# Performance work log

Measured on AMD Instinct MI355X. Metric: run time of the kernel, lower is better.

## Reference

```python
import jax, jax.numpy as jnp
import numpy as np

# Screen config (matches init_kwargs)
W, H, TL = 1920, 1080, 16
NBW = -(-W // TL)          # 120
NBH = -(-H // TL)          # 68
NB = NBW * NBH             # 8160 tiles
N = 500_000                # number of points
K = 5                      # max tiles per axis a point can overlap (radius < 24, TL=16)
RADIUS_MAX = 24.0


def setup_inputs() -> dict:
    key = jax.random.key(0)
    k1, k2, k3 = jax.random.split(key, 3)
    pos2d = jax.random.uniform(k1, (N, 2), dtype=jnp.float32) * jnp.array([W, H], dtype=jnp.float32)
    radius = jax.random.uniform(k2, (N,), dtype=jnp.float32) * (RADIUS_MAX - 1.0) + 1.0
    depth = jax.random.normal(k3, (N,), dtype=jnp.float32)
    return {"pos2d": pos2d, "radius": radius, "depth": depth}


def reference(pos2d, radius, depth):
    # Tile bounds per point (identical clamping semantics to the torch module).
    xmin = jnp.clip(jnp.floor_divide(pos2d[:, 0] - radius, TL), 0, NBW).astype(jnp.int32)
    ymin = jnp.clip(jnp.floor_divide(pos2d[:, 1] - radius, TL), 0, NBH).astype(jnp.int32)
    xmax = jnp.clip(jnp.floor_divide(pos2d[:, 0] + radius, TL) + 1, 0, NBW).astype(jnp.int32)
    ymax = jnp.clip(jnp.floor_divide(pos2d[:, 1] + radius, TL) + 1, 0, NBH).astype(jnp.int32)

    # Enumerate a fixed KxK candidate tile window per point, mask out-of-range tiles.
    dxy = jnp.arange(K, dtype=jnp.int32)
    xi = xmin[:, None] + dxy            # [N, K]
    yi = ymin[:, None] + dxy            # [N, K]
    vx = xi < xmax[:, None]
    vy = yi < ymax[:, None]
    valid = (vx[:, :, None] & vy[:, None, :]).reshape(-1)              # [E]
    tid = (xi[:, :, None] * NBH + yi[:, None, :]).reshape(-1)          # [E] flat tile id (x-major, as in module)
    tid = jnp.where(valid, tid, NB).astype(jnp.int32)                  # sentinel NB -> sorts to end
    pid = jnp.broadcast_to(jnp.arange(N, dtype=jnp.int32)[:, None, None], (N, K, K)).reshape(-1)
    d_entry = jnp.broadcast_to(depth[:, None, None], (N, K, K)).reshape(-1)

    # Counting-sort equivalent: per-tile histogram + exclusive cumsum offsets.
    counts = jax.ops.segment_sum(valid.astype(jnp.int32), tid, num_segments=NB + 1)[:NB]
    tile_count = jnp.concatenate([jnp.zeros((1,), jnp.int32), jnp.cumsum(counts)[:-1].astype(jnp.int32)])

    # Sort pairs by (tile id, depth descending) -> contiguous per-tile, depth-sorted index lists.
    order = jnp.lexsort((-d_entry, tid))
    tid_s = tid[order]
    pid_s = pid[order]
    live = tid_s < NB
    tile_indices = jnp.where(live, pid_s, -1)                          # padded with -1 at the tail
    sorted_depth = jnp.where(live, depth[pid_s], 0.0)                  # depths in per-tile sorted order
    return tile_count, tile_indices, sorted_depth
```

## Files before the change

### kernel.cpp

```cpp
#include <hip/hip_runtime.h>
#include <stdint.h>
#include <math.h>

typedef unsigned short u16;
typedef unsigned int u32;
typedef unsigned long long u64;

#define NBW 120
#define NBH 68
#define NTILES (NBW * NBH)
#define NPTS 500000
#define EE 12500000
#define SORT_CAP 768
#define NBKT 512
#define CAP 128
#define SLABF (NTILES * CAP * 2)
#define HB2 256
#define HT2 1024
#define RD_CH 8
#define RD_WB 17
#define DX 121
#define DY 69
#define DCELLS 8352
#define DCW (DCELLS / 2)

__device__ __forceinline__ int clampi(int v, int lo, int hi) {
    return v < lo ? lo : (v > hi ? hi : v);
}

__device__ __forceinline__ void tile_window(float x, float y, float r,
                                            int& x0, int& x1, int& y0, int& y1) {
    x0 = clampi((int)floorf((x - r) * 0.0625f), 0, NBW);
    x1 = clampi((int)floorf((x + r) * 0.0625f) + 1, 0, NBW);
    y0 = clampi((int)floorf((y - r) * 0.0625f), 0, NBH);
    y1 = clampi((int)floorf((y + r) * 0.0625f) + 1, 0, NBH);
}

__device__ __forceinline__ u32 depth_key(float d) {
    u32 fu = __float_as_uint(d);
    u32 asc = (fu & 0x80000000u) ? ~fu : (fu | 0x80000000u);
    return ~asc;
}
__device__ __forceinline__ float depth_unkey(u32 dk) {
    u32 asc = ~dk;
    u32 fu = (asc & 0x80000000u) ? (asc & 0x7FFFFFFFu) : ~asc;
    return __uint_as_float(fu);
}

__device__ __forceinline__ int tile_of_block(int b) {
    return (b & 7) * (NTILES / 8) + (b >> 3);
}

__device__ __forceinline__ u32 bucket_of(u32 dk, const u32* __restrict__ Ts) {
    u32 k = dk >> 24;
    u32 t0 = Ts[k], t1 = Ts[k + 1];
    u32 b = t0 + (((t1 - t0) * ((dk >> 8) & 0xFFFFu)) >> 16);
    return b >= NBKT ? (NBKT - 1) : b;
}

__device__ __forceinline__ void lds_inc16(u32* arr, int cell) {
    atomicAdd(&arr[cell >> 1], (cell & 1) ? 0x10000u : 1u);
}


__global__ void zero_kernel(u32* __restrict__ cnt, int* __restrict__ sdg) {
    int i = blockIdx.x * 1024 + threadIdx.x;
    if (i < NTILES) cnt[i] = 0;
    int j = i - NTILES;
    if (j >= 0 && j < DCELLS) sdg[j] = 0;
}

__global__ __launch_bounds__(HT2) void scatter_hist_kernel(const float2* __restrict__ pos,
                                                           const float* __restrict__ rad,
                                                           const float* __restrict__ depth,
                                                           u32* __restrict__ cnt,
                                                           u64* __restrict__ slab,
                                                           u32* __restrict__ diffslc) {
    __shared__ u32 s_dp[DCW];
    __shared__ u32 s_dm[DCW];
    int tid = threadIdx.x;
    for (int w = tid; w < DCW; w += HT2) { s_dp[w] = 0; s_dm[w] = 0; }
    __syncthreads();

    for (int i = blockIdx.x * HT2 + tid; i < NPTS; i += HB2 * HT2) {
        float2 p = pos[i];
        float r = rad[i];
        int x0, x1, y0, y1;
        tile_window(p.x, p.y, r, x0, x1, y0, y1);
        int cx = (int)(p.x * 0.0625f);
        int cy = (int)(p.y * 0.0625f);
        u32 dk = depth_key(depth[i]);
        u32 meta = ((u32)(cx - x0) << 11) | ((u32)(x1 - cx - 1) << 9)
                 | ((u32)y0 << 2) | (u32)(y1 - y0 - 1);
        int ct = cx * NBH + cy;
        u32 slot = atomicAdd(&cnt[ct], 1u);
        if (slot < CAP)
            slab[(size_t)ct * CAP + slot] = ((u64)dk << 32) | ((u64)(u32)i << 13) | (u64)meta;
        lds_inc16(s_dp, x0 * DY + y0);
        lds_inc16(s_dp, x1 * DY + y1);
        lds_inc16(s_dm, x0 * DY + y1);
        lds_inc16(s_dm, x1 * DY + y0);
    }
    __syncthreads();

    for (int wi = tid; wi < DCW; wi += HT2) {
        u32 pw = s_dp[wi], mw = s_dm[wi];
        int d0 = (int)(pw & 0xFFFFu) - (int)(mw & 0xFFFFu);
        int d1 = (int)(pw >> 16)     - (int)(mw >> 16);
        diffslc[blockIdx.x * DCW + wi] = ((u32)d0 & 0xFFFFu) | ((u32)d1 << 16);
    }
}

__global__ void reduce_diff_kernel(const u32* __restrict__ diffslc, int* __restrict__ sdg) {
    int chunk = blockIdx.x / RD_WB;
    int wb    = blockIdx.x % RD_WB;
    int wi = wb * 256 + threadIdx.x;
    if (wi >= DCW) return;
    int a0 = 0, a1 = 0;
    int b0 = chunk * (HB2 / RD_CH);
    for (int b = b0; b < b0 + HB2 / RD_CH; ++b) {
        u32 w = diffslc[b * DCW + wi];
        a0 += (int)(short)(w & 0xFFFFu);
        a1 += (int)(short)(w >> 16);
    }
    atomicAdd(&sdg[2 * wi],     a0);
    atomicAdd(&sdg[2 * wi + 1], a1);
}

__global__ __launch_bounds__(1024) void scan2_kernel(const int* __restrict__ sdg,
                                                     u32* __restrict__ eo,
                                                     float* __restrict__ out_count,
                                                     u32* __restrict__ Tg) {
    __shared__ int sd[DCELLS];
    __shared__ u32 wsum16[16];
    __shared__ u32 wpre[17];
    __shared__ u32 traw[257];
    int t = threadIdx.x;
    int lane = t & 63;
    int wvid = t >> 6;

    if (blockIdx.x == 0) {
        for (int c = t; c < DCELLS; c += 1024) sd[c] = sdg[c];
        __syncthreads();

        for (int x = wvid; x < DX; x += 16) {
            int idx = x * DY + lane;
            int v = sd[idx];
            for (int off = 1; off < 64; off <<= 1) {
                int n = __shfl_up(v, off, 64);
                if (lane >= off) v += n;
            }
            sd[idx] = v;
            int carry = __shfl(v, 63, 64);
            int y2 = 64 + lane;
            int v2 = (y2 < DY) ? sd[x * DY + y2] : 0;
            for (int off = 1; off < 64; off <<= 1) {
                int n = __shfl_up(v2, off, 64);
                if (lane >= off) v2 += n;
            }
            if (y2 < DY) sd[x * DY + y2] = v2 + carry;
        }
        __syncthreads();

        for (int y = wvid; y < DY; y += 16) {
            int idx = lane * DY + y;
            int v = sd[idx];
            for (int off = 1; off < 64; off <<= 1) {
                int n = __shfl_up(v, off, 64);
                if (lane >= off) v += n;
            }
            sd[idx] = v;
            int carry = __shfl(v, 63, 64);
            int x2 = 64 + lane;
            int v2 = (x2 < DX) ? sd[x2 * DY + y] : 0;
            for (int off = 1; off < 64; off <<= 1) {
                int n = __shfl_up(v2, off, 64);
                if (lane >= off) v2 += n;
            }
            if (x2 < DX) sd[x2 * DY + y] = v2 + carry;
        }
        __syncthreads();

        int base = t * 8;
        u32 local[8]; u32 sum = 0;
#pragma unroll
        for (int j = 0; j < 8; ++j) {
            int idx = base + j;
            u32 c = 0;
            if (idx < NTILES) {
                int x = idx / NBH, y = idx % NBH;
                c = (u32)sd[x * DY + y];
            }
            local[j] = c; sum += c;
        }
        u32 v = sum;
        for (int off = 1; off < 64; off <<= 1) {
            u32 n = __shfl_up(v, off, 64);
            if (lane >= off) v += n;
        }
        if (lane == 63) wsum16[wvid] = v;
        __syncthreads();
        if (t == 0) {
            u32 run = 0;
            wpre[0] = 0;
#pragma unroll
            for (int w = 0; w < 16; ++w) { run += wsum16[w]; wpre[w + 1] = run; }
        }
        __syncthreads();
        u32 run = wpre[wvid] + v - sum;
#pragma unroll
        for (int j = 0; j < 8; ++j) {
            int idx = base + j;
            if (idx < NTILES) {
                eo[idx] = run;
                out_count[idx] = (float)run;
                run += local[j];
            }
        }
        if (t == 1023) eo[NTILES] = wpre[16];
    } else {
        if (t < 257) {
            u32 dkb = (u32)t << 24;
            float d = depth_unkey(dkb);
            float u;
            if (d != d) u = (t < 128) ? 0.f : 1.f;
            else {
                float dc = fminf(fmaxf(d, -12.f), 12.f);
                u = 0.5f * erfcf(dc * 0.70710678f);
            }
            traw[t] = (u32)(u * (float)NBKT + 0.5f);
        }
        __syncthreads();
        if (t == 0) {
            u32 run = 0;
            for (int k = 0; k < 257; ++k) {
                u32 v = traw[k];
                if (v > NBKT) v = NBKT;
                if (v > run) run = v;
                Tg[k] = run;
            }
        }
    }
}

__global__ __launch_bounds__(256) void tile_build_kernel(const u32* __restrict__ cnt,
                                                         const u64* __restrict__ slab,
                                                         const u32* __restrict__ eo,
                                                         const u32* __restrict__ Tg,
                                                         float* __restrict__ out_idx,
                                                         float* __restrict__ out_depth) {
    __shared__ u64 keys[SORT_CAP];
    __shared__ u64 keys2[SORT_CAP];
    __shared__ u32 boff[NBKT + 1];
    __shared__ u32 bcur[NBKT];
    __shared__ u32 Ts[257];
    __shared__ u32 wsum[4];
    __shared__ u32 lcnt;
    __shared__ u32 nb_n[25];
    __shared__ u32 nb_base[25];
    __shared__ int nb_dcx[25];

    int tid = threadIdx.x;
    int lane = tid & 63;
    int wv = tid >> 6;

    {
        u32 total = eo[NTILES];
        u32 tailn = EE - total;
        u32 per = (tailn + NTILES - 1) / NTILES;
        u64 s = (u64)total + (u64)blockIdx.x * per;
        u64 e = s + per; if (e > (u64)EE) e = EE;
        for (u64 i = s + tid; i < e; i += 256) out_idx[i] = -1.f;

        u32 limit = EE - SLABF;
        u32 tn2 = limit > total ? limit - total : 0;
        u32 per2 = (tn2 + NTILES - 1) / NTILES;
        u64 s2 = (u64)total + (u64)blockIdx.x * per2;
        u64 e2 = s2 + per2; if (e2 > (u64)limit) e2 = limit;
        for (u64 i = s2 + tid; i < e2; i += 256) out_depth[i] = 0.f;
    }

    int t = tile_of_block(blockIdx.x);
    u32 base = eo[t];
    int cnt_e = (int)(eo[t + 1] - base);
    if (cnt_e <= 0) return;

    int tx = t / NBH;
    int ty = t % NBH;
    bool big = cnt_e > SORT_CAP;

    for (int b = tid; b < NBKT; b += 256) boff[b] = 0;
    for (int k = tid; k < 257; k += 256) Ts[k] = Tg[k];
    if (tid == 0) lcnt = 0;
    if (tid < 25) {
        int dx = tid / 5 - 2, dy = tid % 5 - 2;
        int ncx = tx + dx, ncy = ty + dy;
        u32 n = 0, b = 0;
        if (ncx >= 0 && ncx < NBW && ncy >= 0 && ncy < NBH) {
            int nt = ncx * NBH + ncy;
            n = cnt[nt]; if (n > CAP) n = CAP;
            b = (u32)nt * CAP;
        }
        nb_base[tid] = b;
        nb_dcx[tid] = dx;
        nb_n[tid] = n;
    }
    __syncthreads();

    if (!big) {
        for (int k = wv; k < 25; k += 4) {
            u32 n = nb_n[k];
            if (!n) continue;
            const u64* sp = slab + nb_base[k];
            int dcx = nb_dcx[k];
            for (u32 j0 = 0; j0 < n; j0 += 64) {
                u32 j = j0 + lane;
                bool acc = false;
                u64 v = 0;
                if (j < n) {
                    v = sp[j];
                    u32 meta = (u32)v & 0x1FFFu;
                    int h = (int)(meta & 3u);
                    int y0 = (int)((meta >> 2) & 127u);
                    int dx1m1 = (int)((meta >> 9) & 3u);
                    int dx0 = (int)((meta >> 11) & 3u);
                    acc = (dx0 >= dcx && dx1m1 >= -dcx && ty >= y0 && ty <= y0 + h);
                }
                u64 mask = __ballot(acc);
                if (!mask) continue;
                int leader = __ffsll((unsigned long long)mask) - 1;
                u32 nacc = (u32)__popcll(mask);
                u32 wbase = 0;
                if (lane == leader) wbase = atomicAdd(&lcnt, nacc);
                wbase = __shfl(wbase, leader, 64);
                if (acc) {
                    u32 rank = (u32)__popcll(mask & ((1ull << lane) - 1ull));
                    keys[wbase + rank] = v;
                    atomicAdd(&boff[bucket_of((u32)(v >> 32), Ts)], 1u);
                }
            }
        }
        __syncthreads();

        {
            int b0 = tid * 2;
            u32 h0 = boff[b0], h1 = boff[b0 + 1];
            u32 tsum = h0 + h1;
            u32 v = tsum;
            for (int off = 1; off < 64; off <<= 1) {
                u32 n = __shfl_up(v, off, 64);
                if (lane >= off) v += n;
            }
            if (lane == 63) wsum[wv] = v;
            __syncthreads();
            u32 wpre = 0;
            for (int w = 0; w < wv; ++w) wpre += wsum[w];
            u32 run = wpre + v - tsum;
            boff[b0] = run;     bcur[b0] = run;     run += h0;
            boff[b0 + 1] = run; bcur[b0 + 1] = run; run += h1;
            if (tid == 255) boff[NBKT] = run;
        }
        __syncthreads();

        for (int i = tid; i < cnt_e; i += 256) {
            u64 v = keys[i];
            u32 slot = atomicAdd(&bcur[bucket_of((u32)(v >> 32), Ts)], 1u);
            keys2[slot] = v;
        }
        __syncthreads();

        for (int b = tid; b < NBKT; b += 256) {
            int s = (int)boff[b], e = (int)boff[b + 1];
            for (int i = s + 1; i < e; ++i) {
                u64 k = keys2[i];
                int j = i - 1;
                while (j >= s && keys2[j] > k) { keys2[j + 1] = keys2[j]; --j; }
                keys2[j + 1] = k;
            }
        }
        __syncthreads();

        for (int i = tid; i < cnt_e; i += 256) {
            u64 k = keys2[i];
            u32 pid = (u32)(k >> 13) & 0x7FFFFu;
            u32 dk  = (u32)(k >> 32);
            out_idx[base + i]   = (float)pid;
            out_depth[base + i] = depth_unkey(dk);
        }
    } else {
        for (int k = wv; k < 25; k += 4) {
            u32 n = nb_n[k];
            if (!n) continue;
            const u64* sp = slab + nb_base[k];
            int dcx = nb_dcx[k];
            for (u32 j = lane; j < n; j += 64) {
                u64 v = sp[j];
                u32 meta = (u32)v & 0x1FFFu;
                int h = (int)(meta & 3u);
                int y0 = (int)((meta >> 2) & 127u);
                int dx1m1 = (int)((meta >> 9) & 3u);
                int dx0 = (int)((meta >> 11) & 3u);
                if (dx0 >= dcx && dx1m1 >= -dcx && ty >= y0 && ty <= y0 + h) {
                    u32 pid = (u32)(v >> 13) & 0x7FFFFu;
                    u32 dk  = (u32)(v >> 32);
                    u32 slot = atomicAdd(&lcnt, 1u);
                    out_idx[base + slot] = (float)pid;
                    out_depth[base + slot] = depth_unkey(dk);
                }
            }
        }
        __syncthreads();
        for (int round = 0; round < cnt_e; ++round) {
            for (int i = (round & 1) + 2 * tid; i + 1 < cnt_e; i += 512) {
                float fi0 = out_idx[base + i], fi1 = out_idx[base + i + 1];
                float fd0 = out_depth[base + i], fd1 = out_depth[base + i + 1];
                u64 k0 = ((u64)depth_key(fd0) << 19) | (u64)(u32)fi0;
                u64 k1 = ((u64)depth_key(fd1) << 19) | (u64)(u32)fi1;
                if (k0 > k1) {
                    out_idx[base + i] = fi1; out_idx[base + i + 1] = fi0;
                    out_depth[base + i] = fd1; out_depth[base + i + 1] = fd0;
                }
            }
            __syncthreads();
        }
    }
}

__global__ void zero_slab_kernel(float4* __restrict__ dst) {
    int n = SLABF / 4;
    for (int i = blockIdx.x * 256 + threadIdx.x; i < n; i += 512 * 256)
        dst[i] = make_float4(0.f, 0.f, 0.f, 0.f);
}

extern "C" void kernel_launch(void* const* d_in, const int* in_sizes, int n_in,
                              void* d_out, int out_size, void* d_ws, size_t ws_size,
                              hipStream_t stream) {
    (void)in_sizes; (void)n_in; (void)out_size; (void)ws_size;

    const float2* pos  = (const float2*)d_in[0];
    const float* rad   = (const float*)d_in[1];
    const float* depth = (const float*)d_in[2];

    float* out        = (float*)d_out;
    float* out_count  = out;
    float* out_idx    = out + NTILES;
    float* out_depth  = out + NTILES + EE;

    u32* cnt     = (u32*)d_ws;
    u32* eo      = cnt + NTILES;
    int* sdg     = (int*)(eo + NTILES + 1);
    u32* Tg      = (u32*)(sdg + DCELLS);

    u64* slab    = (u64*)(out_depth + EE) - (size_t)NTILES * CAP;
    u32* diffslc = (u32*)(out_idx + EE) - (size_t)HB2 * DCW;

    zero_kernel<<<(NTILES + DCELLS + 1023) / 1024, 1024, 0, stream>>>(cnt, sdg);
    scatter_hist_kernel<<<HB2, HT2, 0, stream>>>(pos, rad, depth, cnt, slab, diffslc);
    reduce_diff_kernel<<<RD_CH * RD_WB, 256, 0, stream>>>(diffslc, sdg);
    scan2_kernel<<<2, 1024, 0, stream>>>(sdg, eo, out_count, Tg);
    tile_build_kernel<<<NTILES, 256, 0, stream>>>(cnt, slab, eo, Tg, out_idx, out_depth);
    zero_slab_kernel<<<512, 256, 0, stream>>>((float4*)(out_depth + EE - SLABF));
}
```

Measured before the change: 207.2 us.

## Move slab to workspace, drop trailing zero pass, widen scatter grid

Places the per-tile key slab in the workspace when it is large enough, so the final zero_slab pass over the output tail can be skipped and tile_build fills the whole depth tail itself. Moves the depth-bucket table computation into the init kernel, which lets the scan kernel run as a single block. Doubles the scatter grid to one point per thread and doubles the reduce chunk count. The result depends on the workspace size, and the diff-slice buffer now takes twice as much space inside the output.

```diff
diff --git a/kernel.cpp b/kernel.cpp
--- a/kernel.cpp
+++ b/kernel.cpp
@@ -14,10 +14,11 @@
 #define SORT_CAP 768
 #define NBKT 512
 #define CAP 128
+#define SLABN ((size_t)NTILES * CAP)
 #define SLABF (NTILES * CAP * 2)
-#define HB2 256
+#define HB2 512
 #define HT2 1024
-#define RD_CH 8
+#define RD_CH 16
 #define RD_WB 17
 #define DX 121
 #define DY 69
@@ -63,11 +64,38 @@
 }
 
 
-__global__ void zero_kernel(u32* __restrict__ cnt, int* __restrict__ sdg) {
-    int i = blockIdx.x * 1024 + threadIdx.x;
-    if (i < NTILES) cnt[i] = 0;
-    int j = i - NTILES;
-    if (j >= 0 && j < DCELLS) sdg[j] = 0;
+__global__ __launch_bounds__(1024) void init_kernel(u32* __restrict__ cnt,
+                                                    int* __restrict__ sdg,
+                                                    u32* __restrict__ Tg) {
+    __shared__ u32 traw[257];
+    int t = threadIdx.x;
+    int gid = blockIdx.x * 1024 + t;
+    if (gid < NTILES) cnt[gid] = 0;
+    else if (gid - NTILES < DCELLS) sdg[gid - NTILES] = 0;
+
+    if (blockIdx.x == 16) {
+        if (t < 257) {
+            u32 dkb = (u32)t << 24;
+            float d = depth_unkey(dkb);
+            float u;
+            if (d != d) u = (t < 128) ? 0.f : 1.f;
+            else {
+                float dc = fminf(fmaxf(d, -12.f), 12.f);
+                u = 0.5f * erfcf(dc * 0.70710678f);
+            }
+            traw[t] = (u32)(u * (float)NBKT + 0.5f);
+        }
+        __syncthreads();
+        if (t == 0) {
+            u32 run = 0;
+            for (int k = 0; k < 257; ++k) {
+                u32 v = traw[k];
+                if (v > NBKT) v = NBKT;
+                if (v > run) run = v;
+                Tg[k] = run;
+            }
+        }
+    }
 }
 
 __global__ __launch_bounds__(HT2) void scatter_hist_kernel(const float2* __restrict__ pos,
@@ -82,7 +110,8 @@
     for (int w = tid; w < DCW; w += HT2) { s_dp[w] = 0; s_dm[w] = 0; }
     __syncthreads();
 
-    for (int i = blockIdx.x * HT2 + tid; i < NPTS; i += HB2 * HT2) {
+    int i = blockIdx.x * HT2 + tid;
+    if (i < NPTS) {
         float2 p = pos[i];
         float r = rad[i];
         int x0, x1, y0, y1;
@@ -127,120 +156,94 @@
     atomicAdd(&sdg[2 * wi + 1], a1);
 }
 
-__global__ __launch_bounds__(1024) void scan2_kernel(const int* __restrict__ sdg,
-                                                     u32* __restrict__ eo,
-                                                     float* __restrict__ out_count,
-                                                     u32* __restrict__ Tg) {
+__global__ __launch_bounds__(1024) void scan_kernel(const int* __restrict__ sdg,
+                                                    u32* __restrict__ eo,
+                                                    float* __restrict__ out_count) {
     __shared__ int sd[DCELLS];
     __shared__ u32 wsum16[16];
     __shared__ u32 wpre[17];
-    __shared__ u32 traw[257];
     int t = threadIdx.x;
     int lane = t & 63;
     int wvid = t >> 6;
 
-    if (blockIdx.x == 0) {
-        for (int c = t; c < DCELLS; c += 1024) sd[c] = sdg[c];
-        __syncthreads();
-
-        for (int x = wvid; x < DX; x += 16) {
-            int idx = x * DY + lane;
-            int v = sd[idx];
-            for (int off = 1; off < 64; off <<= 1) {
-                int n = __shfl_up(v, off, 64);
-                if (lane >= off) v += n;
-            }
-            sd[idx] = v;
-            int carry = __shfl(v, 63, 64);
-            int y2 = 64 + lane;
-            int v2 = (y2 < DY) ? sd[x * DY + y2] : 0;
-            for (int off = 1; off < 64; off <<= 1) {
-                int n = __shfl_up(v2, off, 64);
-                if (lane >= off) v2 += n;
-            }
-            if (y2 < DY) sd[x * DY + y2] = v2 + carry;
-        }
-        __syncthreads();
-
-        for (int y = wvid; y < DY; y += 16) {
-            int idx = lane * DY + y;
-            int v = sd[idx];
-            for (int off = 1; off < 64; off <<= 1) {
-                int n = __shfl_up(v, off, 64);
-                if (lane >= off) v += n;
-            }
-            sd[idx] = v;
-            int carry = __shfl(v, 63, 64);
-            int x2 = 64 + lane;
-            int v2 = (x2 < DX) ? sd[x2 * DY + y] : 0;
-            for (int off = 1; off < 64; off <<= 1) {
-                int n = __shfl_up(v2, off, 64);
-                if (lane >= off) v2 += n;
-            }
-            if (x2 < DX) sd[x2 * DY + y] = v2 + carry;
-        }
-        __syncthreads();
-
-        int base = t * 8;
-        u32 local[8]; u32 sum = 0;
+    for (int c = t; c < DCELLS; c += 1024) sd[c] = sdg[c];
+    __syncthreads();
+
+    for (int x = wvid; x < DX; x += 16) {
+        int idx = x * DY + lane;
+        int v = sd[idx];
+        for (int off = 1; off < 64; off <<= 1) {
+            int n = __shfl_up(v, off, 64);
+            if (lane >= off) v += n;
+        }
+        sd[idx] = v;
+        int carry = __shfl(v, 63, 64);
+        int y2 = 64 + lane;
+        int v2 = (y2 < DY) ? sd[x * DY + y2] : 0;
+        for (int off = 1; off < 64; off <<= 1) {
+            int n = __shfl_up(v2, off, 64);
+            if (lane >= off) v2 += n;
+        }
+        if (y2 < DY) sd[x * DY + y2] = v2 + carry;
+    }
+    __syncthreads();
+
+    for (int y = wvid; y < DY; y += 16) {
+        int idx = lane * DY + y;
+        int v = sd[idx];
+        for (int off = 1; off < 64; off <<= 1) {
+            int n = __shfl_up(v, off, 64);
+            if (lane >= off) v += n;
+        }
+        sd[idx] = v;
+        int carry = __shfl(v, 63, 64);
+        int x2 = 64 + lane;
+        int v2 = (x2 < DX) ? sd[x2 * DY + y] : 0;
+        for (int off = 1; off < 64; off <<= 1) {
+            int n = __shfl_up(v2, off, 64);
+            if (lane >= off) v2 += n;
+        }
+        if (x2 < DX) sd[x2 * DY + y] = v2 + carry;
+    }
+    __syncthreads();
+
+    int base = t * 8;
+    u32 local[8]; u32 sum = 0;
 #pragma unroll
-        for (int j = 0; j < 8; ++j) {
-            int idx = base + j;
-            u32 c = 0;
-            if (idx < NTILES) {
-                int x = idx / NBH, y = idx % NBH;
-                c = (u32)sd[x * DY + y];
-            }
-            local[j] = c; sum += c;
-        }
-        u32 v = sum;
-        for (int off = 1; off < 64; off <<= 1) {
-            u32 n = __shfl_up(v, off, 64);
-            if (lane >= off) v += n;
-        }
-        if (lane == 63) wsum16[wvid] = v;
-        __syncthreads();
-        if (t == 0) {
-            u32 run = 0;
-            wpre[0] = 0;
+    for (int j = 0; j < 8; ++j) {
+        int idx = base + j;
+        u32 c = 0;
+        if (idx < NTILES) {
+            int x = idx / NBH, y = idx % NBH;
+            c = (u32)sd[x * DY + y];
+        }
+        local[j] = c; sum += c;
+    }
+    u32 v = sum;
+    for (int off = 1; off < 64; off <<= 1) {
+        u32 n = __shfl_up(v, off, 64);
+        if (lane >= off) v += n;
+    }
+    if (lane == 63) wsum16[wvid] = v;
+    __syncthreads();
+    if (t == 0) {
+        u32 run = 0;
+        wpre[0] = 0;
 #pragma unroll
-            for (int w = 0; w < 16; ++w) { run += wsum16[w]; wpre[w + 1] = run; }
-        }
-        __syncthreads();
-        u32 run = wpre[wvid] + v - sum;
+        for (int w = 0; w < 16; ++w) { run += wsum16[w]; wpre[w + 1] = run; }
+    }
+    __syncthreads();
+    u32 run = wpre[wvid] + v - sum;
 #pragma unroll
-        for (int j = 0; j < 8; ++j) {
-            int idx = base + j;
-            if (idx < NTILES) {
-                eo[idx] = run;
-                out_count[idx] = (float)run;
-                run += local[j];
-            }
-        }
-        if (t == 1023) eo[NTILES] = wpre[16];
-    } else {
-        if (t < 257) {
-            u32 dkb = (u32)t << 24;
-            float d = depth_unkey(dkb);
-            float u;
-            if (d != d) u = (t < 128) ? 0.f : 1.f;
-            else {
-                float dc = fminf(fmaxf(d, -12.f), 12.f);
-                u = 0.5f * erfcf(dc * 0.70710678f);
-            }
-            traw[t] = (u32)(u * (float)NBKT + 0.5f);
-        }
-        __syncthreads();
-        if (t == 0) {
-            u32 run = 0;
-            for (int k = 0; k < 257; ++k) {
-                u32 v = traw[k];
-                if (v > NBKT) v = NBKT;
-                if (v > run) run = v;
-                Tg[k] = run;
-            }
-        }
-    }
+    for (int j = 0; j < 8; ++j) {
+        int idx = base + j;
+        if (idx < NTILES) {
+            eo[idx] = run;
+            out_count[idx] = (float)run;
+            run += local[j];
+        }
+    }
+    if (t == 1023) eo[NTILES] = wpre[16];
 }
 
 __global__ __launch_bounds__(256) void tile_build_kernel(const u32* __restrict__ cnt,
@@ -248,7 +251,8 @@
                                                          const u32* __restrict__ eo,
                                                          const u32* __restrict__ Tg,
                                                          float* __restrict__ out_idx,
-                                                         float* __restrict__ out_depth) {
+                                                         float* __restrict__ out_depth,
+                                                         u32 depth_fill_end) {
     __shared__ u64 keys[SORT_CAP];
     __shared__ u64 keys2[SORT_CAP];
     __shared__ u32 boff[NBKT + 1];
@@ -272,7 +276,7 @@
         u64 e = s + per; if (e > (u64)EE) e = EE;
         for (u64 i = s + tid; i < e; i += 256) out_idx[i] = -1.f;
 
-        u32 limit = EE - SLABF;
+        u32 limit = depth_fill_end;
         u32 tn2 = limit > total ? limit - total : 0;
         u32 per2 = (tn2 + NTILES - 1) / NTILES;
         u64 s2 = (u64)total + (u64)blockIdx.x * per2;
@@ -435,7 +439,7 @@
 extern "C" void kernel_launch(void* const* d_in, const int* in_sizes, int n_in,
                               void* d_out, int out_size, void* d_ws, size_t ws_size,
                               hipStream_t stream) {
-    (void)in_sizes; (void)n_in; (void)out_size; (void)ws_size;
+    (void)in_sizes; (void)n_in; (void)out_size;
 
     const float2* pos  = (const float2*)d_in[0];
     const float* rad   = (const float*)d_in[1];
@@ -446,18 +450,35 @@
     float* out_idx    = out + NTILES;
     float* out_depth  = out + NTILES + EE;
 
-    u32* cnt     = (u32*)d_ws;
-    u32* eo      = cnt + NTILES;
-    int* sdg     = (int*)(eo + NTILES + 1);
-    u32* Tg      = (u32*)(sdg + DCELLS);
-
-    u64* slab    = (u64*)(out_depth + EE) - (size_t)NTILES * CAP;
+    const size_t small_bytes = (size_t)NTILES * 4
+                             + (size_t)(NTILES + 1) * 4
+                             + (size_t)DCELLS * 4
+                             + 257 * 4;
+    const size_t slab_bytes = SLABN * 8;
+    bool slab_in_ws = ws_size >= slab_bytes + small_bytes;
+
+    u64* slab;
+    u32* cnt;
+    if (slab_in_ws) {
+        slab = (u64*)d_ws;
+        cnt  = (u32*)(slab + SLABN);
+    } else {
+        slab = (u64*)(out_depth + EE) - SLABN;
+        cnt  = (u32*)d_ws;
+    }
+    u32* eo  = cnt + NTILES;
+    int* sdg = (int*)(eo + NTILES + 1);
+    u32* Tg  = (u32*)(sdg + DCELLS);
+
     u32* diffslc = (u32*)(out_idx + EE) - (size_t)HB2 * DCW;
 
-    zero_kernel<<<(NTILES + DCELLS + 1023) / 1024, 1024, 0, stream>>>(cnt, sdg);
+    u32 dfe = slab_in_ws ? (u32)EE : (u32)(EE - SLABF);
+
+    init_kernel<<<17, 1024, 0, stream>>>(cnt, sdg, Tg);
     scatter_hist_kernel<<<HB2, HT2, 0, stream>>>(pos, rad, depth, cnt, slab, diffslc);
     reduce_diff_kernel<<<RD_CH * RD_WB, 256, 0, stream>>>(diffslc, sdg);
-    scan2_kernel<<<2, 1024, 0, stream>>>(sdg, eo, out_count, Tg);
-    tile_build_kernel<<<NTILES, 256, 0, stream>>>(cnt, slab, eo, Tg, out_idx, out_depth);
-    zero_slab_kernel<<<512, 256, 0, stream>>>((float4*)(out_depth + EE - SLABF));
-}
+    scan_kernel<<<1, 1024, 0, stream>>>(sdg, eo, out_count);
+    tile_build_kernel<<<NTILES, 256, 0, stream>>>(cnt, slab, eo, Tg, out_idx, out_depth, dfe);
+    if (!slab_in_ws)
+        zero_slab_kernel<<<512, 256, 0, stream>>>((float4*)(out_depth + EE - SLABF));
+}
```

Measured after the change: 209.5 us. About the same (+1.1%).
